# Kernel tuning notes

Hardware: AMD Instinct MI355X
Metric: run time of the kernel (lower is better)

Reference implementation:

```python
import jax, jax.numpy as jnp
from jax import lax
import numpy as np

D_MODEL = 1024; N_HEADS = 16; D_K = 64; D_FF = 4096
D_STATE = 16; D_CONV = 4; D_INNER = 2048; EPS = 1e-5
BATCH = 2; SEQ = 2048


def _ln(x, g, b):
    m = x.mean(-1, keepdims=True)
    v = ((x - m) ** 2).mean(-1, keepdims=True)
    return (x - m) * lax.rsqrt(v + EPS) * g + b


def setup_inputs() -> dict:
    key = jax.random.key(0)
    ks = jax.random.split(key, 12)
    rn = lambda k, sh, s=0.02: jax.random.normal(k, sh, jnp.float32) * s
    return {
        'x': jax.random.normal(ks[0], (BATCH, SEQ, D_MODEL), jnp.float32),
        'ln1_g': jnp.ones(D_MODEL), 'ln1_b': jnp.zeros(D_MODEL),
        'Wq': rn(ks[1], (D_MODEL, D_MODEL)), 'bq': jnp.zeros(D_MODEL),
        'Wk': rn(ks[2], (D_MODEL, D_MODEL)), 'bk': jnp.zeros(D_MODEL),
        'Wv': rn(ks[3], (D_MODEL, D_MODEL)), 'bv': jnp.zeros(D_MODEL),
        'Wo': rn(ks[4], (D_MODEL, D_MODEL)), 'bo': jnp.zeros(D_MODEL),
        'ln2_g': jnp.ones(D_MODEL), 'ln2_b': jnp.zeros(D_MODEL),
        'in_w': rn(ks[5], (D_MODEL, 2 * D_INNER)), 'in_b': jnp.zeros(2 * D_INNER),
        'conv_w': rn(ks[6], (D_INNER, 1, D_CONV), 0.2), 'conv_b': jnp.zeros(D_INNER),
        'xp_w': rn(ks[7], (D_INNER, 2 * D_STATE)), 'xp_b': jnp.zeros(2 * D_STATE),
        'dt': rn(ks[8], (D_INNER,), 0.1), 'A': rn(ks[9], (D_STATE, D_STATE), 0.1),
        'Dp': jnp.ones(D_INNER),
        'out_w': rn(ks[10], (D_INNER, D_MODEL)), 'out_b': jnp.zeros(D_MODEL),
        'ln3_g': jnp.ones(D_MODEL), 'ln3_b': jnp.zeros(D_MODEL),
        'fc1_w': rn(ks[11], (D_MODEL, D_FF)), 'fc1_b': jnp.zeros(D_FF),
        'fc2_w': rn(jax.random.fold_in(key, 99), (D_FF, D_MODEL)), 'fc2_b': jnp.zeros(D_MODEL),
    }


def reference(x, ln1_g, ln1_b, Wq, bq, Wk, bk, Wv, bv, Wo, bo, ln2_g, ln2_b,
              in_w, in_b, conv_w, conv_b, xp_w, xp_b, dt, A, Dp, out_w, out_b,
              ln3_g, ln3_b, fc1_w, fc1_b, fc2_w, fc2_b):
    Bsz, S, _ = x.shape
    # --- attention (block sliding-window mask == full causal mask) ---
    h = _ln(x, ln1_g, ln1_b)
    q = (h @ Wq + bq).reshape(Bsz, S, N_HEADS, D_K).transpose(0, 2, 1, 3)
    k = (h @ Wk + bk).reshape(Bsz, S, N_HEADS, D_K).transpose(0, 2, 1, 3)
    v = (h @ Wv + bv).reshape(Bsz, S, N_HEADS, D_K).transpose(0, 2, 1, 3)
    scores = jnp.einsum('bhqd,bhkd->bhqk', q, k) / float(D_K ** 0.5)
    causal = jnp.tril(jnp.ones((S, S), bool))
    scores = jnp.where(causal, scores, -jnp.inf)
    probs = jax.nn.softmax(scores, axis=-1)
    attn = jnp.einsum('bhqk,bhkd->bhqd', probs, v).transpose(0, 2, 1, 3).reshape(Bsz, S, D_MODEL)
    x = x + attn @ Wo + bo
    # --- Mamba-style layer ---
    h = _ln(x, ln2_g, ln2_b)
    xr = h @ in_w + in_b                      # (B,S,2*Di)
    xm, res = xr[..., :D_INNER], xr[..., D_INNER:]
    # causal depthwise conv: torch Conv1d(pad=d_conv-1)[..., :S] == left-pad conv
    xc = lax.conv_general_dilated(xm.transpose(0, 2, 1), conv_w, (1,), [(D_CONV - 1, 0)],
                                  dimension_numbers=('NCH', 'OIH', 'NCH'),
                                  feature_group_count=D_INNER)
    xm = jax.nn.silu((xc + conv_b[None, :, None]).transpose(0, 2, 1))
    xdbl = xm @ xp_w + xp_b                   # (B,S,2*d_state)
    Bm, Cm = xdbl[..., :D_STATE], xdbl[..., D_STATE:]
    # dt = exp(param)[:d_state], indexed by i % d_state per step (as in source)
    dts = jnp.exp(dt)[:D_STATE][jnp.arange(S) % D_STATE]  # (S,)
    # NOTE: the source scan never uses u = x[:,i,:] (and hence D); hs depends
    # only on dt, A, B, C — replicated faithfully here.

    def step(hst, inp):
        d_t, b_t, c_t = inp
        A_t = jnp.exp(d_t * A)                # (d_state,d_state)
        hst = jnp.tanh(hst @ A_t.T) + b_t * hst + c_t
        return hst, hst

    h0 = jnp.zeros((Bsz, D_STATE), x.dtype)
    _, hs = lax.scan(step, h0, (dts, Bm.transpose(1, 0, 2), Cm.transpose(1, 0, 2)))
    hs = hs.transpose(1, 0, 2)                # (B,S,d_state)
    y = jnp.repeat(hs, D_INNER // D_STATE, axis=-1) + res
    x = x + y @ out_w + out_b
    # --- FFN (tanh-approx GELU) ---
    h = _ln(x, ln3_g, ln3_b)
    x = x + jax.nn.gelu(h @ fc1_w + fc1_b, approximate=True) @ fc2_w + fc2_b
    return x
```

## Files before the change

kernel.cpp:

```cpp
#include <hip/hip_runtime.h>
#include <hip/hip_bf16.h>


#define SEQ     2048
#define BATCH   2
#define MROWS   4096
#define DMODEL  1024
#define DINNER  2048
#define DFF     4096
#define QKVLD   3072

typedef __attribute__((ext_vector_type(8))) short bf16x8;
typedef __attribute__((ext_vector_type(4))) float f32x4;
typedef __attribute__((ext_vector_type(2))) __fp16 f16x2;

__device__ __forceinline__ unsigned short f2b(float x){
    __hip_bfloat16 h = __float2bfloat16(x);
    return *reinterpret_cast<unsigned short*>(&h);
}
__device__ __forceinline__ float b2f(unsigned short u){
    __hip_bfloat16 h;
    *reinterpret_cast<unsigned short*>(&h) = u;
    return __bfloat162float(h);
}
__device__ __forceinline__ float gelu_f(float v){
    float u = 0.7978845608f*(v + 0.044715f*v*v*v);
    float e = __expf(2.f*u);
    float th = 1.f - 2.f*__builtin_amdgcn_rcpf(e + 1.f);
    return 0.5f*v*(1.f + th);
}
__device__ __forceinline__ void gload16(const unsigned short* g, unsigned short* l){
    __builtin_amdgcn_global_load_lds(
        (const __attribute__((address_space(1))) void*)g,
        (__attribute__((address_space(3))) void*)l, 16, 0, 0);
}
template<int CTRL>
__device__ __forceinline__ float dppf(float x){
    int r = __builtin_amdgcn_mov_dpp(__builtin_bit_cast(int, x), CTRL, 0xf, 0xf, false);
    return __builtin_bit_cast(float, r);
}
template<int CTRL>
__device__ __forceinline__ int dppi(int x){
    return __builtin_amdgcn_mov_dpp(x, CTRL, 0xf, 0xf, false);
}
template<int CTRL>
__device__ __forceinline__ f16x2 dpp_h2(f16x2 x){
    int r = __builtin_amdgcn_mov_dpp(__builtin_bit_cast(int, x), CTRL, 0xf, 0xf, false);
    return __builtin_bit_cast(f16x2, r);
}

#if __has_builtin(__builtin_amdgcn_exp2f)
#define W_SCALE 2.8853900817779268f
__device__ __forceinline__ float exp_2s(float x){ return __builtin_amdgcn_exp2f(x); }
#else
#define W_SCALE 2.0f
__device__ __forceinline__ float exp_2s(float x){ return __expf(x); }
#endif

__device__ __forceinline__ float hdot2(f16x2 a, f16x2 b, float c){
#if __has_builtin(__builtin_amdgcn_fdot2)
    return __builtin_amdgcn_fdot2(a, b, c, false);
#else
    return c + (float)a[0]*(float)b[0] + (float)a[1]*(float)b[1];
#endif
}

__global__ __launch_bounds__(256) void transpose_cast(
    const float* __restrict__ W, unsigned short* __restrict__ Wt, int K, int N)
{
    __shared__ float t[64*65];
    int n0 = blockIdx.x*64, k0 = blockIdx.y*64;
    int c = threadIdx.x & 63, r0 = threadIdx.x >> 6;
    #pragma unroll
    for (int rr = 0; rr < 64; rr += 4)
        t[(rr+r0)*65 + c] = W[(size_t)(k0+rr+r0)*N + n0 + c];
    __syncthreads();
    #pragma unroll
    for (int rr = 0; rr < 64; rr += 4)
        Wt[(size_t)(n0+rr+r0)*K + k0 + c] = f2b(t[c*65 + rr + r0]);
}

__global__ __launch_bounds__(256) void concat_bias(
    const float* __restrict__ b0, const float* __restrict__ b1,
    const float* __restrict__ b2, float* __restrict__ o)
{
    int t = blockIdx.x*256 + threadIdx.x;
    float v = (t < 1024) ? b0[t] : (t < 2048 ? b1[t-1024] : b2[t-2048]);
    o[t] = v;
}

__global__ __launch_bounds__(256) void layernorm_bf16(
    const float* __restrict__ x, const float* __restrict__ g,
    const float* __restrict__ b, unsigned short* __restrict__ out)
{
    int row = blockIdx.x;
    const float4* xr = (const float4*)(x + (size_t)row*DMODEL);
    int tid = threadIdx.x;
    float4 xv = xr[tid];
    float s  = xv.x + xv.y + xv.z + xv.w;
    float ss = xv.x*xv.x + xv.y*xv.y + xv.z*xv.z + xv.w*xv.w;
    #pragma unroll
    for (int d = 32; d > 0; d >>= 1){ s += __shfl_xor(s,d); ss += __shfl_xor(ss,d); }
    __shared__ float sm[8];
    int wv = tid>>6, ln = tid&63;
    if (ln == 0){ sm[wv] = s; sm[4+wv] = ss; }
    __syncthreads();
    s  = sm[0]+sm[1]+sm[2]+sm[3];
    ss = sm[4]+sm[5]+sm[6]+sm[7];
    float mean = s*(1.f/DMODEL);
    float var  = ss*(1.f/DMODEL) - mean*mean;
    float rstd = rsqrtf(var + 1e-5f);
    float4 gv = ((const float4*)g)[tid];
    float4 bv = ((const float4*)b)[tid];
    ushort4 o;
    o.x = f2b((xv.x-mean)*rstd*gv.x + bv.x);
    o.y = f2b((xv.y-mean)*rstd*gv.y + bv.y);
    o.z = f2b((xv.z-mean)*rstd*gv.z + bv.z);
    o.w = f2b((xv.w-mean)*rstd*gv.w + bv.w);
    ((ushort4*)(out + (size_t)row*DMODEL))[tid] = o;
}

template<int BN, int OUT_BF16, int HAS_RES, int ACT>
__global__ __launch_bounds__(256,2) void gemm_bt(
    const unsigned short* __restrict__ A, const unsigned short* __restrict__ Bt,
    const float* __restrict__ bias, const float* __restrict__ res,
    void* __restrict__ outp, int Ndim, int Kdim)
{
    constexpr int NT = BN/32;
    constexpr int BROWS = BN/32;
    __shared__ unsigned short As[128*64];
    __shared__ unsigned short Bs[BN*64];
    int tid = threadIdx.x;
    int lane = tid & 63, wv = tid >> 6;
    int l15 = lane & 15, quad = lane >> 4;
    int m0 = blockIdx.y*128, n0 = blockIdx.x*BN;
    int mo = (wv>>1)*64, no = (wv&1)*(BN/2);
    int rsub = (lane >> 3);
    int cc8  = (lane & 7)*8;
    f32x4 zz = {0.f,0.f,0.f,0.f};
    f32x4 acc[4][NT];
    #pragma unroll
    for (int i=0;i<4;++i)
      #pragma unroll
      for (int j=0;j<NT;++j) acc[i][j] = zz;

    for (int k0 = 0; k0 < Kdim; k0 += 64){
        const unsigned short* Ab = A  + (size_t)(m0 + wv*32 + rsub)*Kdim + k0 + cc8;
        const unsigned short* Bb = Bt + (size_t)(n0 + wv*(BN/4) + rsub)*Kdim + k0 + cc8;
        #pragma unroll
        for (int i=0;i<4;++i)
            gload16(Ab + (size_t)(i*8)*Kdim, &As[(wv*32 + i*8)*64]);
        #pragma unroll
        for (int i=0;i<BROWS;++i)
            gload16(Bb + (size_t)(i*8)*Kdim, &Bs[(wv*(BN/4) + i*8)*64]);
        __syncthreads();
        #pragma unroll
        for (int kc=0;kc<2;++kc){
            bf16x8 af[4], bfr[NT];
            #pragma unroll
            for (int t=0;t<4;++t)
                af[t]  = *(const bf16x8*)(&As[(mo + t*16 + l15)*64 + kc*32 + quad*8]);
            #pragma unroll
            for (int t=0;t<NT;++t)
                bfr[t] = *(const bf16x8*)(&Bs[(no + t*16 + l15)*64 + kc*32 + quad*8]);
            #pragma unroll
            for (int mt=0;mt<4;++mt)
              #pragma unroll
              for (int nt=0;nt<NT;++nt)
                acc[mt][nt] = __builtin_amdgcn_mfma_f32_16x16x32_bf16(af[mt], bfr[nt], acc[mt][nt], 0,0,0);
        }
        __syncthreads();
    }
    #pragma unroll
    for (int mt=0;mt<4;++mt){
      #pragma unroll
      for (int nt=0;nt<NT;++nt){
        int gn = n0 + no + nt*16 + l15;
        float bval = bias[gn];
        #pragma unroll
        for (int r=0;r<4;++r){
            int gm = m0 + mo + mt*16 + quad*4 + r;
            size_t off = (size_t)gm*Ndim + gn;
            float v = acc[mt][nt][r] + bval;
            if constexpr (HAS_RES) v += res[off];
            if constexpr (ACT == 1) v = gelu_f(v);
            if constexpr (OUT_BF16) ((unsigned short*)outp)[off] = f2b(v);
            else                    ((float*)outp)[off] = v;
        }
      }
    }
}

__global__ __launch_bounds__(256) void transpose_v(
    const unsigned short* __restrict__ qkv, unsigned short* __restrict__ vT)
{
    __shared__ unsigned int t[64*33];
    int bh = blockIdx.y;
    int t0 = blockIdx.x*64;
    int tid = threadIdx.x;
    const size_t base = (size_t)(bh>>4)*SEQ*QKVLD + (size_t)(bh&15)*64 + 2*DMODEL;
    #pragma unroll
    for (int i=0;i<2;++i){
        int idx = tid + i*256;
        int r = idx>>3, cc = idx&7;
        uint4 vv = *(const uint4*)(qkv + base + (size_t)(t0+r)*QKVLD + cc*8);
        t[r*33 + cc*4 + 0] = vv.x;
        t[r*33 + cc*4 + 1] = vv.y;
        t[r*33 + cc*4 + 2] = vv.z;
        t[r*33 + cc*4 + 3] = vv.w;
    }
    __syncthreads();
    unsigned short* outb = vT + (size_t)bh*64*SEQ + t0;
    #pragma unroll
    for (int i=0;i<2;++i){
        int idx = tid + i*256;
        int d = idx>>3, cc = idx&7;
        int sh = (d&1)*16, dp = d>>1;
        unsigned int o4[4];
        #pragma unroll
        for (int j2=0;j2<4;++j2){
            unsigned int ua = t[(cc*8 + 2*j2    )*33 + dp];
            unsigned int ub = t[(cc*8 + 2*j2 + 1)*33 + dp];
            unsigned int ha = (ua >> sh) & 0xffff;
            unsigned int hb = (ub >> sh) & 0xffff;
            o4[j2] = ha | (hb << 16);
        }
        *(uint4*)(outb + (size_t)d*SEQ + cc*8) = *(uint4*)o4;
    }
}

__device__ __forceinline__ void stage_kv(
    const unsigned short* __restrict__ k, const unsigned short* __restrict__ vTb,
    int t0, unsigned short* Ks, unsigned short* Vt, int wv, int lane)
{
    #pragma unroll
    for (int p=0;p<4;++p){
        int c0 = p*256 + wv*64;
        int c  = c0 + lane;
        int kr = c>>3, kc = (c&7)*8;
        int vr = c>>4, vc = (c&15)*8;
        gload16(k   + (size_t)(t0+kr)*QKVLD + (kc ^ ((kr&7)<<3)), Ks + c0*8);
        gload16(vTb + (size_t)vr*SEQ + t0 +   (vc ^ ((vr&7)<<3)), Vt + c0*8);
    }
}

__global__ __launch_bounds__(256,3) void attn_flash(
    const unsigned short* __restrict__ qkv, const unsigned short* __restrict__ vT,
    unsigned short* __restrict__ attn)
{
    __shared__ unsigned short Ks[128*64];
    __shared__ unsigned short Vt[64*128];
    __shared__ unsigned short Ps[64*136];
    int bh = blockIdx.y;
    int qt = (int)gridDim.x - 1 - (int)blockIdx.x;
    int q0 = qt*64;
    int tid = threadIdx.x, wv = tid>>6, lane = tid&63;
    int l15 = lane&15, quad = lane>>4;
    int xsw = (l15&7)<<3;
    const size_t basei = (size_t)(bh>>4)*SEQ*QKVLD + (size_t)(bh&15)*64;
    const unsigned short* q = qkv + basei;
    const unsigned short* k = qkv + basei + DMODEL;
    const unsigned short* vTb = vT + (size_t)bh*64*SEQ;
    const size_t baseo = (size_t)(bh>>4)*SEQ*DMODEL + (size_t)(bh&15)*64;

    int nkt = (q0 + 191) >> 7;

    stage_kv(k, vTb, 0, Ks, Vt, wv, lane);

    bf16x8 aq0 = *(const bf16x8*)(q + (size_t)(q0 + wv*16 + l15)*QKVLD + quad*8);
    bf16x8 aq1 = *(const bf16x8*)(q + (size_t)(q0 + wv*16 + l15)*QKVLD + 32 + quad*8);

    float m_i[4], l_i[4];
    f32x4 zz = {0.f,0.f,0.f,0.f};
    f32x4 o[4];
    #pragma unroll
    for (int r=0;r<4;++r){ m_i[r] = -__builtin_inff(); l_i[r] = 0.f; }
    #pragma unroll
    for (int d=0;d<4;++d) o[d] = zz;

    const float SCL = 0.1803368801111137f;

    __syncthreads();

    for (int kt = 0; kt < nkt; ++kt){
        int t0 = kt*128;

        f32x4 sc[8];
        #pragma unroll
        for (int st=0;st<8;++st){
            bf16x8 b0 = *(const bf16x8*)(&Ks[(st*16+l15)*64 + ((     quad*8) ^ xsw)]);
            bf16x8 b1 = *(const bf16x8*)(&Ks[(st*16+l15)*64 + ((32 + quad*8) ^ xsw)]);
            sc[st] = __builtin_amdgcn_mfma_f32_16x16x32_bf16(aq0, b0, zz, 0,0,0);
            sc[st] = __builtin_amdgcn_mfma_f32_16x16x32_bf16(aq1, b1, sc[st], 0,0,0);
        }
        bool diagt = (kt == nkt-1);
        float mrow[4];
        #pragma unroll
        for (int r=0;r<4;++r) mrow[r] = -__builtin_inff();
        #pragma unroll
        for (int st=0;st<8;++st)
          #pragma unroll
          for (int r=0;r<4;++r){
            float svv = sc[st][r]*SCL;
            if (diagt && (t0 + st*16 + l15 > q0 + wv*16 + quad*4 + r))
                svv = -__builtin_inff();
            sc[st][r] = svv;
            mrow[r] = fmaxf(mrow[r], svv);
          }
        #pragma unroll
        for (int d=1; d<16; d<<=1)
          #pragma unroll
          for (int r=0;r<4;++r) mrow[r] = fmaxf(mrow[r], __shfl_xor(mrow[r], d));
        float alpha[4], rsum[4];
        #pragma unroll
        for (int r=0;r<4;++r){
            float mn = fmaxf(m_i[r], mrow[r]);
            alpha[r] = exp_2s(m_i[r] - mn);
            m_i[r] = mn;
        }
        #pragma unroll
        for (int st=0;st<8;++st)
          #pragma unroll
          for (int r=0;r<4;++r) sc[st][r] = exp_2s(sc[st][r] - m_i[r]);
        #pragma unroll
        for (int r=0;r<4;++r){
            rsum[r] = ((sc[0][r]+sc[1][r])+(sc[2][r]+sc[3][r]))
                    + ((sc[4][r]+sc[5][r])+(sc[6][r]+sc[7][r]));
        }
        #pragma unroll
        for (int d=1; d<16; d<<=1)
          #pragma unroll
          for (int r=0;r<4;++r) rsum[r] += __shfl_xor(rsum[r], d);
        #pragma unroll
        for (int r=0;r<4;++r) l_i[r] = l_i[r]*alpha[r] + rsum[r];
        #pragma unroll
        for (int st=0;st<8;++st)
          #pragma unroll
          for (int r=0;r<4;++r)
            Ps[(wv*16 + quad*4 + r)*136 + st*16 + l15] = f2b(sc[st][r]);
        #pragma unroll
        for (int d=0;d<4;++d)
          #pragma unroll
          for (int r=0;r<4;++r) o[d][r] = o[d][r]*alpha[r];

        bf16x8 ap[4];
        #pragma unroll
        for (int kch=0;kch<4;++kch)
            ap[kch] = *(const bf16x8*)(&Ps[(wv*16 + l15)*136 + kch*32 + quad*8]);
        #pragma unroll
        for (int dtile=0;dtile<4;++dtile){
            #pragma unroll
            for (int kch=0;kch<4;++kch){
                bf16x8 bv_ = *(const bf16x8*)(&Vt[(dtile*16+l15)*128 + ((kch*32 + quad*8) ^ xsw)]);
                o[dtile] = __builtin_amdgcn_mfma_f32_16x16x32_bf16(ap[kch], bv_, o[dtile], 0,0,0);
            }
        }

        if (kt + 1 < nkt){
            __syncthreads();
            stage_kv(k, vTb, t0 + 128, Ks, Vt, wv, lane);
            __syncthreads();
        }
    }
    #pragma unroll
    for (int r=0;r<4;++r){
        float inv = 1.f/l_i[r];
        int gm = q0 + wv*16 + quad*4 + r;
        #pragma unroll
        for (int dtile=0;dtile<4;++dtile)
            attn[baseo + (size_t)gm*DMODEL + dtile*16 + l15] = f2b(o[dtile][r]*inv);
    }
}

__global__ __launch_bounds__(256) void conv_silu(
    const unsigned short* __restrict__ xr, const float* __restrict__ cw,
    const float* __restrict__ cb, unsigned short* __restrict__ xm2)
{
    int idx = blockIdx.x*256 + threadIdx.x;
    int r  = idx >> 10;
    int c2 = (idx & 1023)*2;
    int s  = r & (SEQ-1);
    float4 w0 = *(const float4*)(cw + c2*4);
    float4 w1 = *(const float4*)(cw + (c2+1)*4);
    float w0a[4] = {w0.x,w0.y,w0.z,w0.w};
    float w1a[4] = {w1.x,w1.y,w1.z,w1.w};
    float a0 = cb[c2], a1 = cb[c2+1];
    const unsigned short* xrow = xr + (size_t)r*DFF + c2;
    #pragma unroll
    for (int j=0;j<4;++j){
        int sp = s - 3 + j;
        if (sp >= 0){
            int off = (j-3)*DFF;
            unsigned int u = *(const unsigned int*)(xrow + off);
            a0 += w0a[j]*b2f(u & 0xffff);
            a1 += w1a[j]*b2f(u >> 16);
        }
    }
    float s0 = a0 * __builtin_amdgcn_rcpf(1.f + __expf(-a0));
    float s1 = a1 * __builtin_amdgcn_rcpf(1.f + __expf(-a1));
    unsigned int op = (unsigned int)f2b(s0) | ((unsigned int)f2b(s1) << 16);
    *(unsigned int*)(xm2 + (size_t)r*DINNER + c2) = op;
}

__global__ __launch_bounds__(256) void xp_gemm(
    const unsigned short* __restrict__ xm2, const float* __restrict__ w,
    const float* __restrict__ bias, float* __restrict__ xdbl)
{
    int tid = threadIdx.x;
    int lr = tid >> 5, n = tid & 31;
    int row = blockIdx.x*8 + lr;
    const unsigned short* ar = xm2 + (size_t)row*DINNER;
    float acc = bias[n];
    #pragma unroll 4
    for (int k2 = 0; k2 < DINNER; k2 += 2){
        unsigned int u = *(const unsigned int*)(ar + k2);
        acc += b2f(u & 0xffff)*w[k2*32 + n] + b2f(u >> 16)*w[(k2+1)*32 + n];
    }
    int nc = (n < 16) ? 2*n : 2*(n-16)+1;
    xdbl[(size_t)row*32 + nc] = acc;
}

__device__ __forceinline__ float scan_step_dot(float h, const f16x2 (&Wp)[8],
                                               float bv, float cv)
{
    float rr = dppf<0x121>(h);
    f16x2 p0 = __builtin_amdgcn_cvt_pkrtz(h, rr);
    f16x2 p1 = dpp_h2<0x122>(p0);
    f16x2 p2 = dpp_h2<0x124>(p0);
    f16x2 p3 = dpp_h2<0x126>(p0);
    f16x2 p4 = dpp_h2<0x128>(p0);
    f16x2 p5 = dpp_h2<0x12a>(p0);
    f16x2 p6 = dpp_h2<0x12c>(p0);
    f16x2 p7 = dpp_h2<0x12e>(p0);
    float a0 = hdot2(Wp[0], p0, 0.f);
    a0 = hdot2(Wp[1], p1, a0);
    a0 = hdot2(Wp[2], p2, a0);
    a0 = hdot2(Wp[3], p3, a0);
    float a1 = hdot2(Wp[4], p4, 0.f);
    a1 = hdot2(Wp[5], p5, a1);
    a1 = hdot2(Wp[6], p6, a1);
    a1 = hdot2(Wp[7], p7, a1);
    float u  = fmaf(bv, h, cv + 1.f);
    float e2 = exp_2s(a0 + a1);
    float r  = __builtin_amdgcn_rcpf(e2 + 1.f);
    return fmaf(-2.f, r, u);
}

__device__ __forceinline__ void load_bank(float2 (&bk)[16], const float* src){
    #pragma unroll
    for (int j=0;j<16;++j) bk[j] = *(const float2*)(src + (size_t)j*32);
}

__device__ __forceinline__ void compute16(const float2 (&bk)[16],
                                          const f16x2 (&Wf)[16][8],
                                          float& hn, float* hp, int lane)
{
    float h0s=0.f, h1s=0.f, h2s=0.f;
    #pragma unroll
    for (int j=0;j<16;++j){
        hn = scan_step_dot(hn, Wf[j], bk[j].x, bk[j].y);
        if ((j&3)==0)      h0s = hn;
        else if ((j&3)==1) h1s = hn;
        else if ((j&3)==2) h2s = hn;
        else if (lane < 16){
            float4 o4 = {h0s, h1s, h2s, hn};
            *(float4*)(hp + j - 3) = o4;
        }
    }
}

__global__ __launch_bounds__(128,1) void scan_k(
    const float* __restrict__ xdbl, const float* __restrict__ dt,
    const float* __restrict__ A, float* __restrict__ hsT)
{
    int tid = threadIdx.x;
    int lane = tid & 63;
    int b = tid >> 6;
    int i = lane & 15;

    int c1 = dppi<0x121>(i);
    int sj[8], tj[8];
    sj[0] = i;               tj[0] = c1;
    sj[1] = dppi<0x122>(i);  tj[1] = dppi<0x122>(c1);
    sj[2] = dppi<0x124>(i);  tj[2] = dppi<0x124>(c1);
    sj[3] = dppi<0x126>(i);  tj[3] = dppi<0x126>(c1);
    sj[4] = dppi<0x128>(i);  tj[4] = dppi<0x128>(c1);
    sj[5] = dppi<0x12a>(i);  tj[5] = dppi<0x12a>(c1);
    sj[6] = dppi<0x12c>(i);  tj[6] = dppi<0x12c>(c1);
    sj[7] = dppi<0x12e>(i);  tj[7] = dppi<0x12e>(c1);

    f16x2 Wf[16][8];
    #pragma unroll
    for (int p=0;p<16;++p){
        float dtp = __expf(dt[p]);
        #pragma unroll
        for (int jj=0;jj<8;++jj){
            float w0 = W_SCALE*__expf(dtp * A[i*16 + sj[jj]]);
            float w1 = W_SCALE*__expf(dtp * A[i*16 + tj[jj]]);
            Wf[p][jj] = __builtin_amdgcn_cvt_pkrtz(w0, w1);
        }
    }

    const float* src = xdbl + (size_t)(b*SEQ)*32 + 2*i;
    float* hp = hsT + (size_t)(b*16 + i)*SEQ;
    float2 bA[16], bB[16];
    load_bank(bA, src);
    float hn = 0.f;
    for (int bp = 0; bp < 64; ++bp){
        int t0 = bp*32;
        load_bank(bB, src + (size_t)(t0+16)*32);
        compute16(bA, Wf, hn, hp + t0, lane);
        int t2 = (bp < 63) ? (t0 + 32) : 0;
        load_bank(bA, src + (size_t)t2*32);
        compute16(bB, Wf, hn, hp + t0 + 16, lane);
    }
}

__global__ __launch_bounds__(256) void y_assemble(
    const float* __restrict__ hsT, const unsigned short* __restrict__ xr,
    unsigned short* __restrict__ y)
{
    int idx = blockIdx.x*256 + threadIdx.x;
    int r = idx >> 10;
    int c2 = (idx & 1023)*2;
    int bb = r >> 11, s = r & (SEQ-1);
    unsigned int u = *(const unsigned int*)(xr + (size_t)r*DFF + DINNER + c2);
    float h0 = hsT[(size_t)(bb*16 + (c2 >> 7))*SEQ + s];
    float y0 = h0 + b2f(u & 0xffff);
    float y1 = h0 + b2f(u >> 16);
    *(unsigned int*)(y + (size_t)r*DINNER + c2) =
        (unsigned int)f2b(y0) | ((unsigned int)f2b(y1) << 16);
}

extern "C" void kernel_launch(void* const* d_in, const int* in_sizes, int n_in,
                              void* d_out, int out_size, void* d_ws, size_t ws_size,
                              hipStream_t stream)
{
    (void)in_sizes; (void)n_in; (void)out_size; (void)ws_size;
    const float* x     = (const float*)d_in[0];
    const float* ln1_g = (const float*)d_in[1];
    const float* ln1_b = (const float*)d_in[2];
    const float* Wq    = (const float*)d_in[3];
    const float* bq    = (const float*)d_in[4];
    const float* Wk    = (const float*)d_in[5];
    const float* bk    = (const float*)d_in[6];
    const float* Wv    = (const float*)d_in[7];
    const float* bv    = (const float*)d_in[8];
    const float* Wo    = (const float*)d_in[9];
    const float* bo    = (const float*)d_in[10];
    const float* ln2_g = (const float*)d_in[11];
    const float* ln2_b = (const float*)d_in[12];
    const float* in_w  = (const float*)d_in[13];
    const float* in_b  = (const float*)d_in[14];
    const float* conv_w= (const float*)d_in[15];
    const float* conv_b= (const float*)d_in[16];
    const float* xp_w  = (const float*)d_in[17];
    const float* xp_b  = (const float*)d_in[18];
    const float* dt    = (const float*)d_in[19];
    const float* A     = (const float*)d_in[20];
    const float* out_w = (const float*)d_in[22];
    const float* out_b = (const float*)d_in[23];
    const float* ln3_g = (const float*)d_in[24];
    const float* ln3_b = (const float*)d_in[25];
    const float* fc1_w = (const float*)d_in[26];
    const float* fc1_b = (const float*)d_in[27];
    const float* fc2_w = (const float*)d_in[28];
    const float* fc2_b = (const float*)d_in[29];

    char* ws = (char*)d_ws;
    const size_t MB = 1ull << 20;
    unsigned short* qkvT = (unsigned short*)(ws + 0*MB);
    unsigned short* WoT  = (unsigned short*)(ws + 6*MB);
    unsigned short* inT  = (unsigned short*)(ws + 8*MB);
    unsigned short* outT = (unsigned short*)(ws + 16*MB);
    unsigned short* f1T  = (unsigned short*)(ws + 20*MB);
    unsigned short* f2T  = (unsigned short*)(ws + 28*MB);
    unsigned short* hbf  = (unsigned short*)(ws + 36*MB);
    float*          x2   = (float*)(ws + 44*MB);
    float*          x3   = (float*)(ws + 60*MB);
    unsigned short* qkv  = (unsigned short*)(ws + 76*MB);
    unsigned short* attnb= (unsigned short*)(ws + 100*MB);
    unsigned short* xr   = (unsigned short*)(ws + 76*MB);
    unsigned short* ffn  = (unsigned short*)(ws + 76*MB);
    unsigned short* xm2  = (unsigned short*)(ws + 108*MB);
    unsigned short* yb   = (unsigned short*)(ws + 108*MB);
    float*          xdbl = (float*)(ws + 124*MB);
    float*          hsb  = (float*)(ws + 124*MB + 512*1024);
    float*          bqkv = (float*)(ws + 125*MB);

    dim3 blk(256);
    transpose_cast<<<dim3(16,16), blk, 0, stream>>>(Wq, qkvT,              1024, 1024);
    transpose_cast<<<dim3(16,16), blk, 0, stream>>>(Wk, qkvT + 1024*1024,  1024, 1024);
    transpose_cast<<<dim3(16,16), blk, 0, stream>>>(Wv, qkvT + 2*1024*1024,1024, 1024);
    transpose_cast<<<dim3(16,16), blk, 0, stream>>>(Wo, WoT, 1024, 1024);
    transpose_cast<<<dim3(64,16), blk, 0, stream>>>(in_w, inT, 1024, 4096);
    transpose_cast<<<dim3(16,32), blk, 0, stream>>>(out_w, outT, 2048, 1024);
    transpose_cast<<<dim3(64,16), blk, 0, stream>>>(fc1_w, f1T, 1024, 4096);
    transpose_cast<<<dim3(16,64), blk, 0, stream>>>(fc2_w, f2T, 4096, 1024);
    concat_bias<<<12, blk, 0, stream>>>(bq, bk, bv, bqkv);

    layernorm_bf16<<<MROWS, blk, 0, stream>>>(x, ln1_g, ln1_b, hbf);
    gemm_bt<128,1,0,0><<<dim3(24,32), blk, 0, stream>>>(hbf, qkvT, bqkv, nullptr, qkv, QKVLD, 1024);
    transpose_v<<<dim3(32,32), blk, 0, stream>>>(qkv, hbf);
    attn_flash<<<dim3(32,32), blk, 0, stream>>>(qkv, hbf, attnb);
    gemm_bt<64,0,1,0><<<dim3(16,32), blk, 0, stream>>>(attnb, WoT, bo, x, x2, 1024, 1024);
    layernorm_bf16<<<MROWS, blk, 0, stream>>>(x2, ln2_g, ln2_b, hbf);
    gemm_bt<128,1,0,0><<<dim3(32,32), blk, 0, stream>>>(hbf, inT, in_b, nullptr, xr, 4096, 1024);
    conv_silu<<<16384, blk, 0, stream>>>(xr, conv_w, conv_b, xm2);
    xp_gemm<<<512, blk, 0, stream>>>(xm2, xp_w, xp_b, xdbl);
    scan_k<<<1, dim3(128), 0, stream>>>(xdbl, dt, A, hsb);
    y_assemble<<<16384, blk, 0, stream>>>(hsb, xr, yb);
    gemm_bt<64,0,1,0><<<dim3(16,32), blk, 0, stream>>>(yb, outT, out_b, x2, x3, 1024, 2048);
    layernorm_bf16<<<MROWS, blk, 0, stream>>>(x3, ln3_g, ln3_b, hbf);
    gemm_bt<128,1,0,1><<<dim3(32,32), blk, 0, stream>>>(hbf, f1T, fc1_b, nullptr, ffn, 4096, 1024);
    gemm_bt<64,0,1,0><<<dim3(16,32), blk, 0, stream>>>(ffn, f2T, fc2_b, x3, (float*)d_out, 1024, 4096);
}
```

Before: 863.8 us.

## Process 128 query rows per attention block and shorten scan dot chain

The flash-attention kernel now gives each block 128 query rows: each wave handles two 16-row subtiles that share every staged K/V tile, and the grid is halved. This halves K/V global loads and staging barriers per query, at the cost of more registers, so its occupancy hint drops from 3 to 2 blocks. Separately, the GEMM occupancy hint is raised from 2 to 3 blocks per CU. The serial scan's 16-term dot product is now eight independent hdot2 results summed as a tree, which shortens the dependency chain on the latency-bound single-block scan.

New measurement: 891.9 us. 3.3% more time.

```diff
diff --git a/kernel.cpp b/kernel.cpp
--- a/kernel.cpp
+++ b/kernel.cpp
@@ -121,7 +121,7 @@
 }
 
 template<int BN, int OUT_BF16, int HAS_RES, int ACT>
-__global__ __launch_bounds__(256,2) void gemm_bt(
+__global__ __launch_bounds__(256,3) void gemm_bt(
     const unsigned short* __restrict__ A, const unsigned short* __restrict__ Bt,
     const float* __restrict__ bias, const float* __restrict__ res,
     void* __restrict__ outp, int Ndim, int Kdim)
@@ -244,7 +244,7 @@
     }
 }
 
-__global__ __launch_bounds__(256,3) void attn_flash(
+__global__ __launch_bounds__(256,2) void attn_flash(
     const unsigned short* __restrict__ qkv, const unsigned short* __restrict__ vT,
     unsigned short* __restrict__ attn)
 {
@@ -253,7 +253,7 @@
     __shared__ unsigned short Ps[64*136];
     int bh = blockIdx.y;
     int qt = (int)gridDim.x - 1 - (int)blockIdx.x;
-    int q0 = qt*64;
+    int q0 = qt*128;
     int tid = threadIdx.x, wv = tid>>6, lane = tid&63;
     int l15 = lane&15, quad = lane>>4;
     int xsw = (l15&7)<<3;
@@ -263,20 +263,29 @@
     const unsigned short* vTb = vT + (size_t)bh*64*SEQ;
     const size_t baseo = (size_t)(bh>>4)*SEQ*DMODEL + (size_t)(bh&15)*64;
 
-    int nkt = (q0 + 191) >> 7;
+    int nkt = qt + 1;
 
     stage_kv(k, vTb, 0, Ks, Vt, wv, lane);
 
-    bf16x8 aq0 = *(const bf16x8*)(q + (size_t)(q0 + wv*16 + l15)*QKVLD + quad*8);
-    bf16x8 aq1 = *(const bf16x8*)(q + (size_t)(q0 + wv*16 + l15)*QKVLD + 32 + quad*8);
-
-    float m_i[4], l_i[4];
+    bf16x8 aq[2][2];
+    #pragma unroll
+    for (int s=0;s<2;++s){
+        int qr = q0 + wv*32 + s*16 + l15;
+        aq[s][0] = *(const bf16x8*)(q + (size_t)qr*QKVLD + quad*8);
+        aq[s][1] = *(const bf16x8*)(q + (size_t)qr*QKVLD + 32 + quad*8);
+    }
+
+    float m_i[2][4], l_i[2][4];
     f32x4 zz = {0.f,0.f,0.f,0.f};
-    f32x4 o[4];
-    #pragma unroll
-    for (int r=0;r<4;++r){ m_i[r] = -__builtin_inff(); l_i[r] = 0.f; }
-    #pragma unroll
-    for (int d=0;d<4;++d) o[d] = zz;
+    f32x4 o[2][4];
+    #pragma unroll
+    for (int s=0;s<2;++s)
+      #pragma unroll
+      for (int r=0;r<4;++r){ m_i[s][r] = -__builtin_inff(); l_i[s][r] = 0.f; }
+    #pragma unroll
+    for (int s=0;s<2;++s)
+      #pragma unroll
+      for (int d=0;d<4;++d) o[s][d] = zz;
 
     const float SCL = 0.1803368801111137f;
 
@@ -284,75 +293,79 @@
 
     for (int kt = 0; kt < nkt; ++kt){
         int t0 = kt*128;
-
-        f32x4 sc[8];
-        #pragma unroll
-        for (int st=0;st<8;++st){
-            bf16x8 b0 = *(const bf16x8*)(&Ks[(st*16+l15)*64 + ((     quad*8) ^ xsw)]);
-            bf16x8 b1 = *(const bf16x8*)(&Ks[(st*16+l15)*64 + ((32 + quad*8) ^ xsw)]);
-            sc[st] = __builtin_amdgcn_mfma_f32_16x16x32_bf16(aq0, b0, zz, 0,0,0);
-            sc[st] = __builtin_amdgcn_mfma_f32_16x16x32_bf16(aq1, b1, sc[st], 0,0,0);
-        }
-        bool diagt = (kt == nkt-1);
-        float mrow[4];
-        #pragma unroll
-        for (int r=0;r<4;++r) mrow[r] = -__builtin_inff();
-        #pragma unroll
-        for (int st=0;st<8;++st)
-          #pragma unroll
-          for (int r=0;r<4;++r){
-            float svv = sc[st][r]*SCL;
-            if (diagt && (t0 + st*16 + l15 > q0 + wv*16 + quad*4 + r))
-                svv = -__builtin_inff();
-            sc[st][r] = svv;
-            mrow[r] = fmaxf(mrow[r], svv);
-          }
-        #pragma unroll
-        for (int d=1; d<16; d<<=1)
-          #pragma unroll
-          for (int r=0;r<4;++r) mrow[r] = fmaxf(mrow[r], __shfl_xor(mrow[r], d));
-        float alpha[4], rsum[4];
-        #pragma unroll
-        for (int r=0;r<4;++r){
-            float mn = fmaxf(m_i[r], mrow[r]);
-            alpha[r] = exp_2s(m_i[r] - mn);
-            m_i[r] = mn;
-        }
-        #pragma unroll
-        for (int st=0;st<8;++st)
-          #pragma unroll
-          for (int r=0;r<4;++r) sc[st][r] = exp_2s(sc[st][r] - m_i[r]);
-        #pragma unroll
-        for (int r=0;r<4;++r){
-            rsum[r] = ((sc[0][r]+sc[1][r])+(sc[2][r]+sc[3][r]))
-                    + ((sc[4][r]+sc[5][r])+(sc[6][r]+sc[7][r]));
-        }
-        #pragma unroll
-        for (int d=1; d<16; d<<=1)
-          #pragma unroll
-          for (int r=0;r<4;++r) rsum[r] += __shfl_xor(rsum[r], d);
-        #pragma unroll
-        for (int r=0;r<4;++r) l_i[r] = l_i[r]*alpha[r] + rsum[r];
-        #pragma unroll
-        for (int st=0;st<8;++st)
-          #pragma unroll
-          for (int r=0;r<4;++r)
-            Ps[(wv*16 + quad*4 + r)*136 + st*16 + l15] = f2b(sc[st][r]);
-        #pragma unroll
-        for (int d=0;d<4;++d)
-          #pragma unroll
-          for (int r=0;r<4;++r) o[d][r] = o[d][r]*alpha[r];
-
-        bf16x8 ap[4];
-        #pragma unroll
-        for (int kch=0;kch<4;++kch)
-            ap[kch] = *(const bf16x8*)(&Ps[(wv*16 + l15)*136 + kch*32 + quad*8]);
-        #pragma unroll
-        for (int dtile=0;dtile<4;++dtile){
-            #pragma unroll
-            for (int kch=0;kch<4;++kch){
-                bf16x8 bv_ = *(const bf16x8*)(&Vt[(dtile*16+l15)*128 + ((kch*32 + quad*8) ^ xsw)]);
-                o[dtile] = __builtin_amdgcn_mfma_f32_16x16x32_bf16(ap[kch], bv_, o[dtile], 0,0,0);
+        bool diagt = (kt == qt);
+
+        #pragma unroll
+        for (int sub=0; sub<2; ++sub){
+            f32x4 sc[8];
+            #pragma unroll
+            for (int st=0;st<8;++st){
+                bf16x8 b0 = *(const bf16x8*)(&Ks[(st*16+l15)*64 + ((     quad*8) ^ xsw)]);
+                bf16x8 b1 = *(const bf16x8*)(&Ks[(st*16+l15)*64 + ((32 + quad*8) ^ xsw)]);
+                sc[st] = __builtin_amdgcn_mfma_f32_16x16x32_bf16(aq[sub][0], b0, zz, 0,0,0);
+                sc[st] = __builtin_amdgcn_mfma_f32_16x16x32_bf16(aq[sub][1], b1, sc[st], 0,0,0);
+            }
+            int qrb = q0 + wv*32 + sub*16 + quad*4;
+            float mrow[4];
+            #pragma unroll
+            for (int r=0;r<4;++r) mrow[r] = -__builtin_inff();
+            #pragma unroll
+            for (int st=0;st<8;++st)
+              #pragma unroll
+              for (int r=0;r<4;++r){
+                float svv = sc[st][r]*SCL;
+                if (diagt && (t0 + st*16 + l15 > qrb + r))
+                    svv = -__builtin_inff();
+                sc[st][r] = svv;
+                mrow[r] = fmaxf(mrow[r], svv);
+              }
+            #pragma unroll
+            for (int d=1; d<16; d<<=1)
+              #pragma unroll
+              for (int r=0;r<4;++r) mrow[r] = fmaxf(mrow[r], __shfl_xor(mrow[r], d));
+            float alpha[4], rsum[4];
+            #pragma unroll
+            for (int r=0;r<4;++r){
+                float mn = fmaxf(m_i[sub][r], mrow[r]);
+                alpha[r] = exp_2s(m_i[sub][r] - mn);
+                m_i[sub][r] = mn;
+            }
+            #pragma unroll
+            for (int st=0;st<8;++st)
+              #pragma unroll
+              for (int r=0;r<4;++r) sc[st][r] = exp_2s(sc[st][r] - m_i[sub][r]);
+            #pragma unroll
+            for (int r=0;r<4;++r){
+                rsum[r] = ((sc[0][r]+sc[1][r])+(sc[2][r]+sc[3][r]))
+                        + ((sc[4][r]+sc[5][r])+(sc[6][r]+sc[7][r]));
+            }
+            #pragma unroll
+            for (int d=1; d<16; d<<=1)
+              #pragma unroll
+              for (int r=0;r<4;++r) rsum[r] += __shfl_xor(rsum[r], d);
+            #pragma unroll
+            for (int r=0;r<4;++r) l_i[sub][r] = l_i[sub][r]*alpha[r] + rsum[r];
+            #pragma unroll
+            for (int st=0;st<8;++st)
+              #pragma unroll
+              for (int r=0;r<4;++r)
+                Ps[(wv*16 + quad*4 + r)*136 + st*16 + l15] = f2b(sc[st][r]);
+            #pragma unroll
+            for (int d=0;d<4;++d)
+              #pragma unroll
+              for (int r=0;r<4;++r) o[sub][d][r] = o[sub][d][r]*alpha[r];
+
+            bf16x8 ap[4];
+            #pragma unroll
+            for (int kch=0;kch<4;++kch)
+                ap[kch] = *(const bf16x8*)(&Ps[(wv*16 + l15)*136 + kch*32 + quad*8]);
+            #pragma unroll
+            for (int dtile=0;dtile<4;++dtile){
+                #pragma unroll
+                for (int kch=0;kch<4;++kch){
+                    bf16x8 bv_ = *(const bf16x8*)(&Vt[(dtile*16+l15)*128 + ((kch*32 + quad*8) ^ xsw)]);
+                    o[sub][dtile] = __builtin_amdgcn_mfma_f32_16x16x32_bf16(ap[kch], bv_, o[sub][dtile], 0,0,0);
+                }
             }
         }
 
@@ -363,13 +376,15 @@
         }
     }
     #pragma unroll
-    for (int r=0;r<4;++r){
-        float inv = 1.f/l_i[r];
-        int gm = q0 + wv*16 + quad*4 + r;
+    for (int sub=0; sub<2; ++sub)
+      #pragma unroll
+      for (int r=0;r<4;++r){
+        float inv = 1.f/l_i[sub][r];
+        int gm = q0 + wv*32 + sub*16 + quad*4 + r;
         #pragma unroll
         for (int dtile=0;dtile<4;++dtile)
-            attn[baseo + (size_t)gm*DMODEL + dtile*16 + l15] = f2b(o[dtile][r]*inv);
-    }
+            attn[baseo + (size_t)gm*DMODEL + dtile*16 + l15] = f2b(o[sub][dtile][r]*inv);
+      }
 }
 
 __global__ __launch_bounds__(256) void conv_silu(
@@ -432,16 +447,17 @@
     f16x2 p5 = dpp_h2<0x12a>(p0);
     f16x2 p6 = dpp_h2<0x12c>(p0);
     f16x2 p7 = dpp_h2<0x12e>(p0);
-    float a0 = hdot2(Wp[0], p0, 0.f);
-    a0 = hdot2(Wp[1], p1, a0);
-    a0 = hdot2(Wp[2], p2, a0);
-    a0 = hdot2(Wp[3], p3, a0);
-    float a1 = hdot2(Wp[4], p4, 0.f);
-    a1 = hdot2(Wp[5], p5, a1);
-    a1 = hdot2(Wp[6], p6, a1);
-    a1 = hdot2(Wp[7], p7, a1);
+    float d0 = hdot2(Wp[0], p0, 0.f);
+    float d1 = hdot2(Wp[1], p1, 0.f);
+    float d2 = hdot2(Wp[2], p2, 0.f);
+    float d3 = hdot2(Wp[3], p3, 0.f);
+    float d4 = hdot2(Wp[4], p4, 0.f);
+    float d5 = hdot2(Wp[5], p5, 0.f);
+    float d6 = hdot2(Wp[6], p6, 0.f);
+    float d7 = hdot2(Wp[7], p7, 0.f);
+    float x  = ((d0+d1)+(d2+d3)) + ((d4+d5)+(d6+d7));
     float u  = fmaf(bv, h, cv + 1.f);
-    float e2 = exp_2s(a0 + a1);
+    float e2 = exp_2s(x);
     float r  = __builtin_amdgcn_rcpf(e2 + 1.f);
     return fmaf(-2.f, r, u);
 }
@@ -602,7 +618,7 @@
     layernorm_bf16<<<MROWS, blk, 0, stream>>>(x, ln1_g, ln1_b, hbf);
     gemm_bt<128,1,0,0><<<dim3(24,32), blk, 0, stream>>>(hbf, qkvT, bqkv, nullptr, qkv, QKVLD, 1024);
     transpose_v<<<dim3(32,32), blk, 0, stream>>>(qkv, hbf);
-    attn_flash<<<dim3(32,32), blk, 0, stream>>>(qkv, hbf, attnb);
+    attn_flash<<<dim3(16,32), blk, 0, stream>>>(qkv, hbf, attnb);
     gemm_bt<64,0,1,0><<<dim3(16,32), blk, 0, stream>>>(attnb, WoT, bo, x, x2, 1024, 1024);
     layernorm_bf16<<<MROWS, blk, 0, stream>>>(x2, ln2_g, ln2_b, hbf);
     gemm_bt<128,1,0,0><<<dim3(32,32), blk, 0, stream>>>(hbf, inT, in_b, nullptr, xr, 4096, 1024);
```
